# Kernel optimization log

Measured on AMD Instinct MI355X. Metric: run time of the kernel, lower is better.

## Reference

```python
import jax, jax.numpy as jnp
import numpy as np

B, S, H, NH, NKV, HD, E, I = 1, 2048, 1024, 16, 8, 64, 8, 2048
TOPK = 2
EPS = 1e-6
THETA = 1e6


def setup_inputs() -> dict:
    key = jax.random.key(0)
    ks = jax.random.split(key, 12)
    init = lambda k, shp: jax.random.normal(k, shp, jnp.float32) * 0.02
    hidden_states = jax.random.normal(ks[0], (B, S, H), jnp.float32)
    attention_mask = jnp.ones((B, S), jnp.float32)
    position_ids = jnp.broadcast_to(jnp.arange(S, dtype=jnp.int32), (B, S))
    inv_freq = 1.0 / (THETA ** (jnp.arange(0, HD, 2, dtype=jnp.float32) / HD))
    freqs = jnp.outer(jnp.arange(S, dtype=jnp.float32), inv_freq)  # [S, HD/2]
    emb = jnp.concatenate([freqs, freqs], axis=-1)                  # [S, HD]
    return dict(
        hidden_states=hidden_states,
        attention_mask=attention_mask,
        position_ids=position_ids,
        sin=jnp.sin(emb), cos=jnp.cos(emb),
        wq=init(ks[1], (H, NH * HD)),
        wk=init(ks[2], (H, NKV * HD)),
        wv=init(ks[3], (H, NKV * HD)),
        wo=init(ks[4], (NH * HD, H)),
        ln1=jnp.ones((H,), jnp.float32),
        ln2=jnp.ones((H,), jnp.float32),
        gate_w=init(ks[5], (H, E)),
        w1=init(ks[6], (E, H, I)),
        w3=init(ks[7], (E, H, I)),
        w2=init(ks[8], (E, I, H)),
    )


def _rms_norm(x, w):
    return x * jax.lax.rsqrt(jnp.mean(jnp.square(x), -1, keepdims=True) + EPS) * w


def _rotate_half(x):
    h = x.shape[-1] // 2
    return jnp.concatenate([-x[..., h:], x[..., :h]], axis=-1)


def reference(hidden_states, attention_mask, position_ids, sin, cos,
              wq, wk, wv, wo, ln1, ln2, gate_w, w1, w3, w2):
    x = hidden_states
    # ---- self-attention block ----
    h = _rms_norm(x, ln1)
    q = (h @ wq).reshape(B, S, NH, HD).transpose(0, 2, 1, 3)    # [B,NH,S,HD]
    k = (h @ wk).reshape(B, S, NKV, HD).transpose(0, 2, 1, 3)   # [B,NKV,S,HD]
    v = (h @ wv).reshape(B, S, NKV, HD).transpose(0, 2, 1, 3)
    sb = sin[position_ids][:, None]  # [B,1,S,HD]
    cb = cos[position_ids][:, None]
    q = q * cb + _rotate_half(q) * sb
    k = k * cb + _rotate_half(k) * sb
    rep = NH // NKV
    k = jnp.repeat(k, rep, axis=1)  # GQA repeat -> [B,NH,S,HD]
    v = jnp.repeat(v, rep, axis=1)
    causal = jnp.tril(jnp.ones((S, S), bool))
    mask = causal[None, None] & (attention_mask[:, None, None, :] > 0)
    bias = jnp.where(mask, 0.0, jnp.finfo(jnp.float32).min)
    scale = 1.0 / jnp.sqrt(jnp.float32(HD))
    scores = jnp.einsum('bhqd,bhkd->bhqk', q, k) * scale + bias
    attn = jax.nn.softmax(scores, axis=-1)
    o = jnp.einsum('bhqk,bhkd->bhqd', attn, v)
    o = o.transpose(0, 2, 1, 3).reshape(B, S, NH * HD) @ wo
    x = x + o
    # ---- sparse MoE block (top-2 of E experts, SiLU-gated MLP) ----
    t = _rms_norm(x, ln2).reshape(B * S, H)
    router_logits = t @ gate_w                         # [T,E]
    probs = jax.nn.softmax(router_logits, axis=-1)
    top_w, top_i = jax.lax.top_k(probs, TOPK)          # [T,2]
    top_w = top_w / jnp.sum(top_w, axis=-1, keepdims=True)
    full_w = jnp.sum(jax.nn.one_hot(top_i, E, dtype=t.dtype) * top_w[..., None], axis=1)  # [T,E]
    moe_out = jnp.zeros_like(t)
    for e in range(E):  # fixed small expert count
        ge = jax.nn.silu(t @ w1[e]) * (t @ w3[e])      # [T,I]
        moe_out = moe_out + full_w[:, e:e + 1] * (ge @ w2[e])
    x = x + moe_out.reshape(B, S, H)
    return x
```

## Files before the change

### kernel.cpp

```cpp
#include <hip/hip_runtime.h>

#define S 2048
#define H 1024
#define NH 16
#define NKV 8
#define HD 64
#define NE 8
#define ID 2048

typedef short bf16x8 __attribute__((ext_vector_type(8)));
typedef short bf16x4 __attribute__((ext_vector_type(4)));
typedef float f32x4 __attribute__((ext_vector_type(4)));

__device__ __forceinline__ unsigned short f2bf(float f) {
  unsigned u = __builtin_bit_cast(unsigned, f);
  u += 0x7FFFu + ((u >> 16) & 1u);
  return (unsigned short)(u >> 16);
}
__device__ __forceinline__ float bf2f(unsigned short h) {
  unsigned u = ((unsigned)h) << 16;
  return __builtin_bit_cast(float, u);
}
__device__ __forceinline__ unsigned cvtpk(float a, float b) {
  unsigned r;
  asm("v_cvt_pk_bf16_f32 %0, %1, %2" : "=v"(r) : "v"(a), "v"(b));
  return r;
}

typedef const __attribute__((address_space(1))) unsigned int gas_u32;
typedef __attribute__((address_space(3))) unsigned int las_u32;
__device__ __forceinline__ void gload16(const unsigned short* g, unsigned short* l) {
  __builtin_amdgcn_global_load_lds((gas_u32*)g, (las_u32*)l, 16, 0, 0);
}

__global__ __launch_bounds__(256) void rmsnorm_kernel(const float* __restrict__ x,
                                                      const float* __restrict__ wgt,
                                                      unsigned short* __restrict__ ohi,
                                                      unsigned short* __restrict__ olo) {
  int row = blockIdx.x;
  const float* xr = x + (size_t)row * H;
  int tid = threadIdx.x;
  float v[4];
  float ss = 0.f;
#pragma unroll
  for (int i = 0; i < 4; i++) {
    v[i] = xr[tid + i * 256];
    ss += v[i] * v[i];
  }
#pragma unroll
  for (int off = 1; off < 64; off <<= 1) ss += __shfl_xor(ss, off);
  __shared__ float part[4];
  if ((tid & 63) == 0) part[tid >> 6] = ss;
  __syncthreads();
  float tot = part[0] + part[1] + part[2] + part[3];
  float r = rsqrtf(tot * (1.f / H) + 1e-6f);
#pragma unroll
  for (int i = 0; i < 4; i++) {
    int c = tid + i * 256;
    float vv = v[i] * r * wgt[c];
    size_t o = (size_t)row * H + c;
    unsigned short h_ = f2bf(vv);
    ohi[o] = h_;
    olo[o] = f2bf(vv - bf2f(h_));
  }
}

__global__ __launch_bounds__(256) void rmsnorm_router_kernel(
    const float* __restrict__ x, const float* __restrict__ wgt,
    const float* __restrict__ gw, unsigned short* __restrict__ ohi,
    int* __restrict__ selE, float* __restrict__ selW) {
  int row = blockIdx.x;
  const float* xr = x + (size_t)row * H;
  int tid = threadIdx.x;
  float v[4];
  float ss = 0.f;
#pragma unroll
  for (int i = 0; i < 4; i++) {
    v[i] = xr[tid + i * 256];
    ss += v[i] * v[i];
  }
#pragma unroll
  for (int off = 1; off < 64; off <<= 1) ss += __shfl_xor(ss, off);
  __shared__ float part[4];
  __shared__ float red[4][NE];
  if ((tid & 63) == 0) part[tid >> 6] = ss;
  __syncthreads();
  float tot = part[0] + part[1] + part[2] + part[3];
  float r = rsqrtf(tot * (1.f / H) + 1e-6f);
  float acc[NE];
#pragma unroll
  for (int e = 0; e < NE; e++) acc[e] = 0.f;
#pragma unroll
  for (int i = 0; i < 4; i++) {
    int c = tid + i * 256;
    float vv = v[i] * r * wgt[c];
    ohi[(size_t)row * H + c] = f2bf(vv);
    const float4* gp = (const float4*)(gw + (size_t)c * NE);
    float4 g0 = gp[0], g1 = gp[1];
    acc[0] += vv * g0.x;
    acc[1] += vv * g0.y;
    acc[2] += vv * g0.z;
    acc[3] += vv * g0.w;
    acc[4] += vv * g1.x;
    acc[5] += vv * g1.y;
    acc[6] += vv * g1.z;
    acc[7] += vv * g1.w;
  }
#pragma unroll
  for (int off = 1; off < 64; off <<= 1) {
#pragma unroll
    for (int e = 0; e < NE; e++) acc[e] += __shfl_xor(acc[e], off);
  }
  if ((tid & 63) == 0) {
#pragma unroll
    for (int e = 0; e < NE; e++) red[tid >> 6][e] = acc[e];
  }
  __syncthreads();
  if (tid == 0) {
    float lg[NE];
#pragma unroll
    for (int e = 0; e < NE; e++) lg[e] = red[0][e] + red[1][e] + red[2][e] + red[3][e];
    int e1 = 0;
#pragma unroll
    for (int e = 1; e < NE; e++)
      if (lg[e] > lg[e1]) e1 = e;
    int e2 = -1;
#pragma unroll
    for (int e = 0; e < NE; e++)
      if (e != e1 && (e2 < 0 || lg[e] > lg[e2])) e2 = e;
    float w1v = 1.f / (1.f + __expf(lg[e2] - lg[e1]));
    selE[row] = e1 | (e2 << 8);
    selW[row * 2] = w1v;
    selW[row * 2 + 1] = 1.f - w1v;
  }
}

__global__ __launch_bounds__(256) void assign_kernel(const int* __restrict__ selE,
                                                     const float* __restrict__ selW,
                                                     int* __restrict__ cnt,
                                                     int* __restrict__ offs,
                                                     int* __restrict__ tmap,
                                                     int* __restrict__ idxb,
                                                     float* __restrict__ wgtb) {
  int tid = threadIdx.x;
  __shared__ int sc[256][NE];
  int pack[8];
  int hist[NE];
#pragma unroll
  for (int e = 0; e < NE; e++) hist[e] = 0;
#pragma unroll
  for (int i = 0; i < 8; i++) {
    pack[i] = selE[tid * 8 + i];
    hist[pack[i] & 255]++;
    hist[(pack[i] >> 8) & 255]++;
  }
#pragma unroll
  for (int e = 0; e < NE; e++) sc[tid][e] = hist[e];
  __syncthreads();
  for (int off = 1; off < 256; off <<= 1) {
    int add[NE];
    bool has = tid >= off;
    if (has) {
#pragma unroll
      for (int e = 0; e < NE; e++) add[e] = sc[tid - off][e];
    }
    __syncthreads();
    if (has) {
#pragma unroll
      for (int e = 0; e < NE; e++) sc[tid][e] += add[e];
    }
    __syncthreads();
  }
  if (tid == 0) {
    int a = 0, t = 0;
    for (int e = 0; e < NE; e++) {
      int totE = sc[255][e];
      offs[e] = a;
      cnt[e] = totE;
      int nt = (totE + 127) >> 7;
      for (int i = 0; i < nt; i++) tmap[t++] = (e << 16) | i;
      a += totE;
    }
    offs[NE] = a;
    tmap[63] = t;
  }
  int run[NE];
#pragma unroll
  for (int e = 0; e < NE; e++) run[e] = sc[tid][e] - hist[e];
#pragma unroll
  for (int i = 0; i < 8; i++) {
    int tok = tid * 8 + i;
    int e1 = pack[i] & 255, e2 = (pack[i] >> 8) & 255;
    float wa = selW[tok * 2], wb = selW[tok * 2 + 1];
    int p1 = run[e1]++;
    idxb[e1 * S + p1] = tok;
    wgtb[e1 * S + p1] = wa;
    int p2 = run[e2]++;
    idxb[e2 * S + p2] = tok;
    wgtb[e2 * S + p2] = wb;
  }
}

template <bool LO>
__global__ __launch_bounds__(256) void tconv_kernel(const float* __restrict__ src,
                                                    unsigned short* __restrict__ hi,
                                                    unsigned short* __restrict__ lo,
                                                    int K, int N, long long sStride,
                                                    long long dStride) {
  int nt = blockIdx.x, kt = blockIdx.y, b = blockIdx.z;
  src += (size_t)b * sStride;
  hi += (size_t)b * dStride;
  if (LO) lo += (size_t)b * dStride;
  __shared__ float tile[64][65];
  int tid = threadIdx.x;
  int r = tid >> 2, cs = (tid & 3) * 16;
  const float* s0 = src + (size_t)(kt * 64 + r) * N + nt * 64 + cs;
#pragma unroll
  for (int i = 0; i < 16; i += 4) {
    float4 a = *(const float4*)(s0 + i);
    tile[r][cs + i] = a.x;
    tile[r][cs + i + 1] = a.y;
    tile[r][cs + i + 2] = a.z;
    tile[r][cs + i + 3] = a.w;
  }
  __syncthreads();
  int n = nt * 64 + r;
  size_t dbase = (size_t)n * K + kt * 64 + cs;
  unsigned short th[16], tl[16];
#pragma unroll
  for (int i = 0; i < 16; i++) {
    float vv = tile[cs + i][r];
    unsigned short h_ = f2bf(vv);
    th[i] = h_;
    if (LO) tl[i] = f2bf(vv - bf2f(h_));
  }
  *(bf16x8*)(hi + dbase) = *(bf16x8*)&th[0];
  *(bf16x8*)(hi + dbase + 8) = *(bf16x8*)&th[8];
  if (LO) {
    *(bf16x8*)(lo + dbase) = *(bf16x8*)&tl[0];
    *(bf16x8*)(lo + dbase + 8) = *(bf16x8*)&tl[8];
  }
}

template <int MODE>
__global__ __launch_bounds__(256, (MODE >= 2 ? 4 : 3)) void gemm_kernel(
    const unsigned short* __restrict__ Ah, const unsigned short* __restrict__ Al,
    const unsigned short* __restrict__ Bh, const unsigned short* __restrict__ Bl,
    float* __restrict__ C, float* __restrict__ C2, unsigned short* __restrict__ Gout,
    const float* __restrict__ resid, const int* __restrict__ idx,
    const float* __restrict__ wgt, const int* __restrict__ cnt,
    const int* __restrict__ offs, const int* __restrict__ tmap, int N, int K) {
  int n0 = blockIdx.x * 64, m0, e = 0;
  int ce = 0, gbase = 0;
  if (MODE >= 2) {
    int ntiles = tmap[63];
    if ((int)blockIdx.y >= ntiles) return;
    int packed = tmap[blockIdx.y];
    e = packed >> 16;
    m0 = (packed & 0xffff) * 128;
    ce = cnt[e];
    gbase = offs[e];
  } else {
    m0 = blockIdx.y * 128;
  }
  const unsigned short* bhp = Bh;
  const unsigned short* blp = Bl;
  if (MODE == 2) {
    bhp += (size_t)e * 2048 * 1024;
    blp += (size_t)e * 2048 * 1024;
  }
  if (MODE == 3) bhp += (size_t)e * 1024 * 2048;

  __shared__ __align__(16) unsigned short tAh[128 * 64];
  __shared__ __align__(16) unsigned short tAl[MODE <= 1 ? 128 * 64 : 8];
  __shared__ __align__(16) unsigned short tBh[64 * 64];
  __shared__ __align__(16) unsigned short tBl[MODE <= 2 ? 64 * 64 : 8];

  int tid = threadIdx.x, w = tid >> 6, lane = tid & 63;
  int lr = lane & 15, g = lane >> 4;
  int rloc = lane >> 3, slotg = (lane & 7) ^ rloc;
  int wm = w >> 1, wn = w & 1;

  unsigned aOff[4], bOff[2];
#pragma unroll
  for (int cc = 0; cc < 4; cc++) {
    int rr = w * 32 + cc * 8 + rloc;
    if (MODE == 2) {
      int gr = m0 + rr;
      if (gr > ce - 1) gr = ce - 1;
      int tok = idx[e * S + gr];
      aOff[cc] = (unsigned)(tok * K + slotg * 8);
    } else if (MODE == 3) {
      int gr = gbase + m0 + rr;
      if (gr > 4095) gr = 4095;
      aOff[cc] = (unsigned)(gr * K + slotg * 8);
    } else {
      aOff[cc] = (unsigned)((m0 + rr) * K + slotg * 8);
    }
  }
#pragma unroll
  for (int cc = 0; cc < 2; cc++) {
    int rr = w * 16 + cc * 8 + rloc;
    bOff[cc] = (unsigned)((n0 + rr) * K + slotg * 8);
  }

  f32x4 acc[4][2], acc2[4][2];
#pragma unroll
  for (int i = 0; i < 4; i++)
#pragma unroll
    for (int j = 0; j < 2; j++) {
      acc[i][j] = f32x4{0.f, 0.f, 0.f, 0.f};
      if (MODE == 2) acc2[i][j] = f32x4{0.f, 0.f, 0.f, 0.f};
    }

  int kbeg = 0, kend = K;
  if (MODE == 3) {
    kbeg = (int)blockIdx.z * (K >> 1);
    kend = kbeg + (K >> 1);
  }
  for (int k0 = kbeg; k0 < kend; k0 += 64) {
    __syncthreads();
#pragma unroll
    for (int cc = 0; cc < 4; cc++) {
      int cb = (w * 4 + cc) * 512;
      gload16(Ah + aOff[cc] + k0, &tAh[cb]);
      if (MODE <= 1) gload16(Al + aOff[cc] + k0, &tAl[cb]);
    }
#pragma unroll
    for (int cc = 0; cc < 2; cc++) {
      int cb = (w * 2 + cc) * 512;
      gload16(bhp + bOff[cc] + k0, &tBh[cb]);
      if (MODE <= 2) gload16(blp + bOff[cc] + k0, &tBl[cb]);
    }
    __syncthreads();
    bf16x8 fah[4][2], fal[4][2];
#pragma unroll
    for (int i = 0; i < 4; i++) {
      int ar = wm * 64 + i * 16 + lr;
#pragma unroll
      for (int kk = 0; kk < 2; kk++) {
        int off = ar * 64 + (((kk * 4 + g) ^ (ar & 7)) * 8);
        fah[i][kk] = *(const bf16x8*)&tAh[off];
        if (MODE <= 1) fal[i][kk] = *(const bf16x8*)&tAl[off];
      }
    }
#pragma unroll
    for (int j = 0; j < 2; j++) {
      int br = wn * 32 + j * 16 + lr;
      bf16x8 fbh[2], fbl[2];
#pragma unroll
      for (int kk = 0; kk < 2; kk++) {
        int off = br * 64 + (((kk * 4 + g) ^ (br & 7)) * 8);
        fbh[kk] = *(const bf16x8*)&tBh[off];
        if (MODE <= 2) fbl[kk] = *(const bf16x8*)&tBl[off];
      }
#pragma unroll
      for (int i = 0; i < 4; i++) {
#pragma unroll
        for (int kk = 0; kk < 2; kk++) {
          acc[i][j] = __builtin_amdgcn_mfma_f32_16x16x32_bf16(fah[i][kk], fbh[kk], acc[i][j], 0, 0, 0);
          if (MODE <= 1) {
            acc[i][j] = __builtin_amdgcn_mfma_f32_16x16x32_bf16(fah[i][kk], fbl[kk], acc[i][j], 0, 0, 0);
            acc[i][j] = __builtin_amdgcn_mfma_f32_16x16x32_bf16(fal[i][kk], fbh[kk], acc[i][j], 0, 0, 0);
          }
          if (MODE == 2)
            acc2[i][j] = __builtin_amdgcn_mfma_f32_16x16x32_bf16(fah[i][kk], fbl[kk], acc2[i][j], 0, 0, 0);
        }
      }
    }
  }
#pragma unroll
  for (int i = 0; i < 4; i++)
#pragma unroll
    for (int j = 0; j < 2; j++)
#pragma unroll
      for (int r = 0; r < 4; r++) {
        int grow = wm * 64 + i * 16 + g * 4 + r;
        int gcol = n0 + wn * 32 + j * 16 + lr;
        float v = acc[i][j][r];
        if (MODE == 0) {
          C[(size_t)(m0 + grow) * N + gcol] = v;
        } else if (MODE == 1) {
          float o = v + resid[(size_t)(m0 + grow) * N + gcol];
          C[(size_t)(m0 + grow) * N + gcol] = o;
          C2[(size_t)(m0 + grow) * N + gcol] = o;
        } else if (MODE == 2) {
          if (m0 + grow < ce) {
            float g3 = acc2[i][j][r];
            float sg = v / (1.f + __expf(-v));
            Gout[(size_t)(gbase + m0 + grow) * 2048 + gcol] = f2bf(sg * g3);
          }
        } else {
          if (m0 + grow < ce) {
            int tok = idx[e * S + m0 + grow];
            float wv = wgt[e * S + m0 + grow];
            atomicAdd(&C[(size_t)tok * 1024 + gcol], v * wv);
          }
        }
      }
}

__global__ __launch_bounds__(256) void rope_kernel(
    const float* __restrict__ qkv, const float* __restrict__ sinb,
    const float* __restrict__ cosb, const int* __restrict__ pos,
    unsigned short* __restrict__ qhi, unsigned short* __restrict__ qlo,
    unsigned short* __restrict__ khi, unsigned short* __restrict__ klo) {
  int i = blockIdx.x * 256 + threadIdx.x;
  int d = i & 31;
  int s = (i >> 5) & 2047;
  int hh = i >> 16;
  int p = pos[s];
  float c0 = cosb[p * HD + d], c1 = cosb[p * HD + d + 32];
  float s0 = sinb[p * HD + d], s1 = sinb[p * HD + d + 32];
  const float* srcb = qkv + (size_t)s * 2048;
  if (hh < NH) {
    float x0 = srcb[hh * HD + d], x1 = srcb[hh * HD + d + 32];
    float r0 = (x0 * c0 - x1 * s0) * 0.125f;
    float r1 = (x1 * c1 + x0 * s1) * 0.125f;
    size_t o = ((size_t)hh * S + s) * HD + d;
    unsigned short h0 = f2bf(r0), h1 = f2bf(r1);
    qhi[o] = h0;
    qlo[o] = f2bf(r0 - bf2f(h0));
    qhi[o + 32] = h1;
    qlo[o + 32] = f2bf(r1 - bf2f(h1));
  } else {
    int hk = hh - NH;
    float x0 = srcb[1024 + hk * HD + d], x1 = srcb[1024 + hk * HD + d + 32];
    float r0 = x0 * c0 - x1 * s0;
    float r1 = x1 * c1 + x0 * s1;
    size_t o = ((size_t)hk * S + s) * HD + d;
    unsigned short h0 = f2bf(r0), h1 = f2bf(r1);
    khi[o] = h0;
    klo[o] = f2bf(r0 - bf2f(h0));
    khi[o + 32] = h1;
    klo[o + 32] = f2bf(r1 - bf2f(h1));
  }
}

__global__ __launch_bounds__(256) void vtrans_kernel(const float* __restrict__ qkv,
                                                     unsigned short* __restrict__ vThi,
                                                     unsigned short* __restrict__ vTlo) {
  int st = blockIdx.x, hk = blockIdx.y;
  __shared__ float tile[64][65];
  int tid = threadIdx.x;
  int r = tid >> 2, seg = (tid & 3) * 16;
  const float* src = qkv + (size_t)(st * 64 + r) * 2048 + 1536 + hk * HD + seg;
#pragma unroll
  for (int i = 0; i < 16; i += 4) {
    float4 a = *(const float4*)(src + i);
    tile[r][seg + i] = a.x;
    tile[r][seg + i + 1] = a.y;
    tile[r][seg + i + 2] = a.z;
    tile[r][seg + i + 3] = a.w;
  }
  __syncthreads();
  int d = tid >> 2, ss = (tid & 3) * 16;
  unsigned short th[16], tl[16];
#pragma unroll
  for (int i = 0; i < 16; i++) {
    float vv = tile[ss + i][d];
    unsigned short h_ = f2bf(vv);
    th[i] = h_;
    tl[i] = f2bf(vv - bf2f(h_));
  }
  size_t dst = ((size_t)hk * HD + d) * S + st * 64 + ss;
  *(bf16x8*)(vThi + dst) = *(bf16x8*)&th[0];
  *(bf16x8*)(vThi + dst + 8) = *(bf16x8*)&th[8];
  *(bf16x8*)(vTlo + dst) = *(bf16x8*)&tl[0];
  *(bf16x8*)(vTlo + dst + 8) = *(bf16x8*)&tl[8];
}

#define FSWZ(row, byteoff) ((byteoff) ^ (((row) & 7) << 4))

__global__ __launch_bounds__(256, 4) void flash_kernel(
    const unsigned short* __restrict__ qhi, const unsigned short* __restrict__ qlo,
    const unsigned short* __restrict__ khip, const unsigned short* __restrict__ klop,
    const unsigned short* __restrict__ vthip, const unsigned short* __restrict__ vtlop,
    const float* __restrict__ amask, float* __restrict__ po, float* __restrict__ pm,
    float* __restrict__ pl) {
  int u = blockIdx.x;
  int r_ = u >> 8, base = u & 255;
  int qt = (base + r_ * 8) & 31;
  int head = ((base >> 5) & 7) | ((r_ & 1) << 3);
  int z = r_ >> 1;
  int tid = threadIdx.x;
  int w = tid >> 6, lane = tid & 63;
  int lr = lane & 15, g = lane >> 4;
  int rloc = lane >> 3, slotg = (lane & 7) ^ rloc;

  __shared__ __align__(16) unsigned short Khi[64 * 64];
  __shared__ __align__(16) unsigned short Klo[64 * 64];
  __shared__ __align__(16) unsigned short Vhi[64 * 64];
  __shared__ __align__(16) unsigned short Vlo[64 * 64];
  __shared__ __align__(16) unsigned short Pbuf[4][16 * 64];

  int qrow = qt * 64 + w * 16 + lr;
  bf16x8 qh[2], ql[2];
  {
    const unsigned short* qb = qhi + ((size_t)head * S + qrow) * HD;
    const unsigned short* qb2 = qlo + ((size_t)head * S + qrow) * HD;
    qh[0] = *(const bf16x8*)(qb + g * 8);
    qh[1] = *(const bf16x8*)(qb + 32 + g * 8);
    ql[0] = *(const bf16x8*)(qb2 + g * 8);
    ql[1] = *(const bf16x8*)(qb2 + 32 + g * 8);
  }

  f32x4 oacc[4];
#pragma unroll
  for (int dg = 0; dg < 4; dg++) oacc[dg] = f32x4{0.f, 0.f, 0.f, 0.f};
  float m = -1e30f, l = 0.f;

  const unsigned short* kbh = khip + (size_t)(head >> 1) * S * HD;
  const unsigned short* kbl = klop + (size_t)(head >> 1) * S * HD;
  const unsigned short* vbh = vthip + (size_t)(head >> 1) * HD * S;
  const unsigned short* vbl = vtlop + (size_t)(head >> 1) * HD * S;
  char* pbase = (char*)Pbuf[w];

  int nblk = qt + 1;
  int b0 = (z * nblk) >> 1, b1 = ((z + 1) * nblk) >> 1;

  for (int kb = b0; kb < b1; kb++) {
    int kv0 = kb * 64;
    __syncthreads();
#pragma unroll
    for (int cc = 0; cc < 2; cc++) {
      int c = w * 2 + cc;
      int r = c * 8 + rloc;
      gload16(kbh + (size_t)(kv0 + r) * HD + slotg * 8, &Khi[c * 512]);
      gload16(kbl + (size_t)(kv0 + r) * HD + slotg * 8, &Klo[c * 512]);
      gload16(vbh + (size_t)r * S + kv0 + slotg * 8, &Vhi[c * 512]);
      gload16(vbl + (size_t)r * S + kv0 + slotg * 8, &Vlo[c * 512]);
    }
    unsigned long long vm = __ballot(amask[kv0 + lane] > 0.f);
    __syncthreads();

    f32x4 sacc[4];
#pragma unroll
    for (int c = 0; c < 4; c++) sacc[c] = f32x4{0.f, 0.f, 0.f, 0.f};
#pragma unroll
    for (int c = 0; c < 4; c++) {
#pragma unroll
      for (int kc = 0; kc < 2; kc++) {
        int row = c * 16 + lr;
        int bo = FSWZ(row, row * 128 + kc * 64 + g * 16);
        bf16x8 khf = *(const bf16x8*)((char*)Khi + bo);
        bf16x8 klf = *(const bf16x8*)((char*)Klo + bo);
        sacc[c] = __builtin_amdgcn_mfma_f32_16x16x32_bf16(khf, qh[kc], sacc[c], 0, 0, 0);
        sacc[c] = __builtin_amdgcn_mfma_f32_16x16x32_bf16(khf, ql[kc], sacc[c], 0, 0, 0);
        sacc[c] = __builtin_amdgcn_mfma_f32_16x16x32_bf16(klf, qh[kc], sacc[c], 0, 0, 0);
      }
    }
    int qloc = w * 16 + lr;
    bool diag = (kb == qt);
    bool fullvis = (vm == ~0ull) && !diag;
    float tm = -1e30f;
    if (fullvis) {
#pragma unroll
      for (int c = 0; c < 4; c++)
#pragma unroll
        for (int r = 0; r < 4; r++) tm = fmaxf(tm, sacc[c][r]);
    } else {
#pragma unroll
      for (int c = 0; c < 4; c++) {
#pragma unroll
        for (int r = 0; r < 4; r++) {
          int kvloc = c * 16 + 4 * g + r;
          bool vis = ((vm >> kvloc) & 1ull) && (!diag || kvloc <= qloc);
          float sv = vis ? sacc[c][r] : -1e30f;
          sacc[c][r] = sv;
          tm = fmaxf(tm, sv);
        }
      }
    }
    tm = fmaxf(tm, __shfl_xor(tm, 16));
    tm = fmaxf(tm, __shfl_xor(tm, 32));
    bool skip = __all(tm - m <= 8.f);
    float newm = skip ? m : fmaxf(m, tm);
    float rs = 0.f;
#pragma unroll
    for (int c = 0; c < 4; c++) {
#pragma unroll
      for (int r = 0; r < 4; r++) {
        float p = __expf(sacc[c][r] - newm);
        sacc[c][r] = p;
        rs += p;
      }
    }
    rs += __shfl_xor(rs, 16);
    rs += __shfl_xor(rs, 32);
    if (!skip) {
      float alpha = __expf(m - newm);
      m = newm;
      l = l * alpha + rs;
#pragma unroll
      for (int dg = 0; dg < 4; dg++) {
#pragma unroll
        for (int r = 0; r < 4; r++) oacc[dg][r] *= alpha;
      }
    } else {
      l += rs;
    }
    unsigned hw[4][2];
#pragma unroll
    for (int c = 0; c < 4; c++) {
      hw[c][0] = cvtpk(sacc[c][0], sacc[c][1]);
      hw[c][1] = cvtpk(sacc[c][2], sacc[c][3]);
      uint2 hv = {hw[c][0], hw[c][1]};
      *(uint2*)(pbase + FSWZ(lr, lr * 128 + (c * 16 + 4 * g) * 2)) = hv;
    }
    bf16x8 pbh[2], pbl[2];
#pragma unroll
    for (int kc = 0; kc < 2; kc++)
      pbh[kc] = *(const bf16x8*)(pbase + FSWZ(lr, lr * 128 + kc * 64 + g * 16));
#pragma unroll
    for (int c = 0; c < 4; c++) {
      float h0 = __builtin_bit_cast(float, hw[c][0] << 16);
      float h1 = __builtin_bit_cast(float, hw[c][0] & 0xffff0000u);
      float h2 = __builtin_bit_cast(float, hw[c][1] << 16);
      float h3 = __builtin_bit_cast(float, hw[c][1] & 0xffff0000u);
      uint2 lv = {cvtpk(sacc[c][0] - h0, sacc[c][1] - h1),
                  cvtpk(sacc[c][2] - h2, sacc[c][3] - h3)};
      *(uint2*)(pbase + FSWZ(lr, lr * 128 + (c * 16 + 4 * g) * 2)) = lv;
    }
#pragma unroll
    for (int kc = 0; kc < 2; kc++)
      pbl[kc] = *(const bf16x8*)(pbase + FSWZ(lr, lr * 128 + kc * 64 + g * 16));
#pragma unroll
    for (int dg = 0; dg < 4; dg++) {
#pragma unroll
      for (int kc = 0; kc < 2; kc++) {
        int row = dg * 16 + lr;
        int bo = FSWZ(row, row * 128 + kc * 64 + g * 16);
        bf16x8 vhf = *(const bf16x8*)((char*)Vhi + bo);
        bf16x8 vlf = *(const bf16x8*)((char*)Vlo + bo);
        oacc[dg] = __builtin_amdgcn_mfma_f32_16x16x32_bf16(vhf, pbh[kc], oacc[dg], 0, 0, 0);
        oacc[dg] = __builtin_amdgcn_mfma_f32_16x16x32_bf16(vhf, pbl[kc], oacc[dg], 0, 0, 0);
        oacc[dg] = __builtin_amdgcn_mfma_f32_16x16x32_bf16(vlf, pbh[kc], oacc[dg], 0, 0, 0);
      }
    }
  }

  size_t pb = (size_t)(qt * 16 + head) * 2 + z;
  int row = w * 16 + lr;
  if (g == 0) {
    pm[pb * 64 + row] = m;
    pl[pb * 64 + row] = l;
  }
  float* pob = po + pb * 4096 + (size_t)row * 64;
#pragma unroll
  for (int dg = 0; dg < 4; dg++) {
    float4 v4 = {oacc[dg][0], oacc[dg][1], oacc[dg][2], oacc[dg][3]};
    *(float4*)(pob + dg * 16 + 4 * g) = v4;
  }
}

__global__ __launch_bounds__(256) void combine_kernel(const float* __restrict__ po,
                                                      const float* __restrict__ pm,
                                                      const float* __restrict__ pl,
                                                      unsigned short* __restrict__ ohi,
                                                      unsigned short* __restrict__ olo) {
  int qt = blockIdx.x, head = blockIdx.y;
  int r = threadIdx.x >> 2, dg = (threadIdx.x & 3) * 16;
  size_t base = (size_t)(qt * 16 + head) * 2;
  float m0v = pm[base * 64 + r], m1v = pm[(base + 1) * 64 + r];
  float l0 = pl[base * 64 + r], l1 = pl[(base + 1) * 64 + r];
  float M = fmaxf(m0v, m1v);
  float w0 = __expf(m0v - M), w1 = __expf(m1v - M);
  float inv = 1.f / (w0 * l0 + w1 * l1);
  const float* p0 = po + base * 4096 + (size_t)r * 64 + dg;
  const float* p1 = po + (base + 1) * 4096 + (size_t)r * 64 + dg;
  unsigned short th[16], tl[16];
#pragma unroll
  for (int i = 0; i < 16; i += 4) {
    float4 a = *(const float4*)(p0 + i);
    float4 b = *(const float4*)(p1 + i);
    float vv[4] = {(w0 * a.x + w1 * b.x) * inv, (w0 * a.y + w1 * b.y) * inv,
                   (w0 * a.z + w1 * b.z) * inv, (w0 * a.w + w1 * b.w) * inv};
#pragma unroll
    for (int j = 0; j < 4; j++) {
      unsigned short h_ = f2bf(vv[j]);
      th[i + j] = h_;
      tl[i + j] = f2bf(vv[j] - bf2f(h_));
    }
  }
  size_t ob = (size_t)(qt * 64 + r) * 1024 + head * 64 + dg;
  *(bf16x8*)(ohi + ob) = *(bf16x8*)&th[0];
  *(bf16x8*)(ohi + ob + 8) = *(bf16x8*)&th[8];
  *(bf16x8*)(olo + ob) = *(bf16x8*)&tl[0];
  *(bf16x8*)(olo + ob + 8) = *(bf16x8*)&tl[8];
}

extern "C" void kernel_launch(void* const* d_in, const int* in_sizes, int n_in,
                              void* d_out, int out_size, void* d_ws, size_t ws_size,
                              hipStream_t stream) {
  const float* x = (const float*)d_in[0];
  const float* amask = (const float*)d_in[1];
  const int* pos = (const int*)d_in[2];
  const float* sinb = (const float*)d_in[3];
  const float* cosb = (const float*)d_in[4];
  const float* wq = (const float*)d_in[5];
  const float* wk = (const float*)d_in[6];
  const float* wv = (const float*)d_in[7];
  const float* wo = (const float*)d_in[8];
  const float* ln1 = (const float*)d_in[9];
  const float* ln2 = (const float*)d_in[10];
  const float* gw = (const float*)d_in[11];
  const float* w1 = (const float*)d_in[12];
  const float* w3 = (const float*)d_in[13];
  const float* w2 = (const float*)d_in[14];
  float* out = (float*)d_out;

  char* ws = (char*)d_ws;
  const size_t MB = 1024 * 1024;
  float* x2 = (float*)(ws + 0 * MB);
  unsigned short* t_bf = (unsigned short*)(ws + 8 * MB);
  int* cnt = (int*)(ws + 12 * MB);
  int* offs = cnt + 16;
  int* tmap = cnt + 32;
  int* idxb = cnt + 128;
  float* wgtb = (float*)(idxb + NE * S);
  unsigned short* G = (unsigned short*)(ws + 13 * MB);
  unsigned short* w1T = (unsigned short*)(ws + 29 * MB);
  unsigned short* w3T = (unsigned short*)(ws + 61 * MB);
  unsigned short* w2T = (unsigned short*)(ws + 29 * MB);
  float* qkv = (float*)(ws + 13 * MB);
  float* po = (float*)(ws + 13 * MB);
  unsigned short* wqkvT_hi = (unsigned short*)(ws + 29 * MB);
  unsigned short* wqkvT_lo = (unsigned short*)(ws + 33 * MB);
  unsigned short* woT_hi = (unsigned short*)(ws + 37 * MB);
  unsigned short* woT_lo = (unsigned short*)(ws + 39 * MB);
  unsigned short* h_hi = (unsigned short*)(ws + 41 * MB);
  unsigned short* h_lo = (unsigned short*)(ws + 45 * MB);
  unsigned short* q_hi = (unsigned short*)(ws + 49 * MB);
  unsigned short* q_lo = (unsigned short*)(ws + 53 * MB);
  unsigned short* k_hi = (unsigned short*)(ws + 57 * MB);
  unsigned short* k_lo = (unsigned short*)(ws + 59 * MB);
  unsigned short* vT_hi = (unsigned short*)(ws + 61 * MB);
  unsigned short* vT_lo = (unsigned short*)(ws + 63 * MB);
  unsigned short* o_hi = (unsigned short*)(ws + 65 * MB);
  unsigned short* o_lo = (unsigned short*)(ws + 69 * MB);
  float* pm = (float*)(ws + 81 * MB);
  float* pl = (float*)(ws + 82 * MB);
  int* selE = (int*)(ws + 83 * MB);
  float* selW = (float*)(ws + 84 * MB);

  rmsnorm_kernel<<<S, 256, 0, stream>>>(x, ln1, h_hi, h_lo);
  tconv_kernel<true><<<dim3(16, 16, 1), 256, 0, stream>>>(wq, wqkvT_hi, wqkvT_lo, 1024, 1024, 0, 0);
  tconv_kernel<true><<<dim3(8, 16, 1), 256, 0, stream>>>(wk, wqkvT_hi + (size_t)1024 * 1024,
                                                         wqkvT_lo + (size_t)1024 * 1024, 1024, 512, 0, 0);
  tconv_kernel<true><<<dim3(8, 16, 1), 256, 0, stream>>>(wv, wqkvT_hi + (size_t)1536 * 1024,
                                                         wqkvT_lo + (size_t)1536 * 1024, 1024, 512, 0, 0);
  tconv_kernel<true><<<dim3(16, 16, 1), 256, 0, stream>>>(wo, woT_hi, woT_lo, 1024, 1024, 0, 0);

  gemm_kernel<0><<<dim3(32, 16, 1), 256, 0, stream>>>(h_hi, h_lo, wqkvT_hi, wqkvT_lo, qkv, nullptr,
                                                      nullptr, nullptr, nullptr, nullptr, nullptr,
                                                      nullptr, nullptr, 2048, 1024);
  rope_kernel<<<6144, 256, 0, stream>>>(qkv, sinb, cosb, pos, q_hi, q_lo, k_hi, k_lo);
  vtrans_kernel<<<dim3(32, 8), 256, 0, stream>>>(qkv, vT_hi, vT_lo);
  flash_kernel<<<dim3(1024, 1, 1), 256, 0, stream>>>(q_hi, q_lo, k_hi, k_lo, vT_hi, vT_lo, amask,
                                                     po, pm, pl);
  combine_kernel<<<dim3(32, 16), 256, 0, stream>>>(po, pm, pl, o_hi, o_lo);
  gemm_kernel<1><<<dim3(16, 16, 1), 256, 0, stream>>>(o_hi, o_lo, woT_hi, woT_lo, x2, out, nullptr,
                                                      x, nullptr, nullptr, nullptr, nullptr,
                                                      nullptr, 1024, 1024);
  rmsnorm_router_kernel<<<S, 256, 0, stream>>>(x2, ln2, gw, t_bf, selE, selW);
  assign_kernel<<<1, 256, 0, stream>>>(selE, selW, cnt, offs, tmap, idxb, wgtb);

  tconv_kernel<false><<<dim3(32, 16, 8), 256, 0, stream>>>(w1, w1T, nullptr, 1024, 2048,
                                                           (long long)1024 * 2048,
                                                           (long long)2048 * 1024);
  tconv_kernel<false><<<dim3(32, 16, 8), 256, 0, stream>>>(w3, w3T, nullptr, 1024, 2048,
                                                           (long long)1024 * 2048,
                                                           (long long)2048 * 1024);
  gemm_kernel<2><<<dim3(32, 40, 1), 256, 0, stream>>>(t_bf, nullptr, w1T, w3T, nullptr, nullptr, G,
                                                      nullptr, idxb, wgtb, cnt, offs, tmap, 2048,
                                                      1024);
  tconv_kernel<false><<<dim3(16, 32, 8), 256, 0, stream>>>(w2, w2T, nullptr, 2048, 1024,
                                                           (long long)2048 * 1024,
                                                           (long long)1024 * 2048);
  gemm_kernel<3><<<dim3(16, 40, 2), 256, 0, stream>>>(G, nullptr, w2T, nullptr, out, nullptr,
                                                      nullptr, nullptr, idxb, wgtb, cnt, offs, tmap,
                                                      1024, 2048);
}
```

Before: 307.3 us.

## Replace MoE down-proj atomics with slot-indexed partial stores and gather; halve dense GEMM M-tile

The expert down-projection GEMM no longer scatters weighted results into the output with float atomicAdd. It writes unweighted partial results per split-K half into a slot-ordered buffer, and a new gather kernel combines both experts and both K-halves per token, applying the routing weights. The assign kernel now records each token's slot positions instead of per-slot weights. Separately, the dense QKV and output-projection GEMMs use a 64-row M tile with doubled grid and 4-wave occupancy, which adds blocks to improve CU utilisation. The trade-off is an extra kernel launch and a 32MB intermediate buffer round trip in place of the atomic contention.

```diff
diff --git a/kernel.cpp b/kernel.cpp
--- a/kernel.cpp
+++ b/kernel.cpp
@@ -136,12 +136,11 @@
 }
 
 __global__ __launch_bounds__(256) void assign_kernel(const int* __restrict__ selE,
-                                                     const float* __restrict__ selW,
                                                      int* __restrict__ cnt,
                                                      int* __restrict__ offs,
                                                      int* __restrict__ tmap,
                                                      int* __restrict__ idxb,
-                                                     float* __restrict__ wgtb) {
+                                                     int* __restrict__ tokslot) {
   int tid = threadIdx.x;
   __shared__ int sc[256][NE];
   int pack[8];
@@ -171,17 +170,25 @@
     }
     __syncthreads();
   }
+  int offsL[NE];
+  {
+    int a = 0;
+#pragma unroll
+    for (int e = 0; e < NE; e++) {
+      offsL[e] = a;
+      a += sc[255][e];
+    }
+  }
   if (tid == 0) {
-    int a = 0, t = 0;
+    int t = 0;
     for (int e = 0; e < NE; e++) {
       int totE = sc[255][e];
-      offs[e] = a;
+      offs[e] = offsL[e];
       cnt[e] = totE;
       int nt = (totE + 127) >> 7;
       for (int i = 0; i < nt; i++) tmap[t++] = (e << 16) | i;
-      a += totE;
-    }
-    offs[NE] = a;
+    }
+    offs[NE] = offsL[NE - 1] + sc[255][NE - 1];
     tmap[63] = t;
   }
   int run[NE];
@@ -191,14 +198,36 @@
   for (int i = 0; i < 8; i++) {
     int tok = tid * 8 + i;
     int e1 = pack[i] & 255, e2 = (pack[i] >> 8) & 255;
-    float wa = selW[tok * 2], wb = selW[tok * 2 + 1];
     int p1 = run[e1]++;
     idxb[e1 * S + p1] = tok;
-    wgtb[e1 * S + p1] = wa;
     int p2 = run[e2]++;
     idxb[e2 * S + p2] = tok;
-    wgtb[e2 * S + p2] = wb;
-  }
+    tokslot[tok * 2] = offsL[e1] + p1;
+    tokslot[tok * 2 + 1] = offsL[e2] + p2;
+  }
+}
+
+__global__ __launch_bounds__(256) void moe_gather_kernel(const float* __restrict__ moeP,
+                                                         const int* __restrict__ tokslot,
+                                                         const float* __restrict__ selW,
+                                                         float* __restrict__ out) {
+  int tok = blockIdx.x;
+  int c = threadIdx.x * 4;
+  int s0 = tokslot[tok * 2], s1 = tokslot[tok * 2 + 1];
+  float w0 = selW[tok * 2], w1 = selW[tok * 2 + 1];
+  const float* P0 = moeP;
+  const float* P1 = moeP + (size_t)4096 * 1024;
+  float4 a0 = *(const float4*)(P0 + (size_t)s0 * 1024 + c);
+  float4 b0 = *(const float4*)(P1 + (size_t)s0 * 1024 + c);
+  float4 a1 = *(const float4*)(P0 + (size_t)s1 * 1024 + c);
+  float4 b1 = *(const float4*)(P1 + (size_t)s1 * 1024 + c);
+  float* op = out + (size_t)tok * 1024 + c;
+  float4 o = *(float4*)op;
+  o.x += w0 * (a0.x + b0.x) + w1 * (a1.x + b1.x);
+  o.y += w0 * (a0.y + b0.y) + w1 * (a1.y + b1.y);
+  o.z += w0 * (a0.z + b0.z) + w1 * (a1.z + b1.z);
+  o.w += w0 * (a0.w + b0.w) + w1 * (a1.w + b1.w);
+  *(float4*)op = o;
 }
 
 template <bool LO>
@@ -243,13 +272,15 @@
 }
 
 template <int MODE>
-__global__ __launch_bounds__(256, (MODE >= 2 ? 4 : 3)) void gemm_kernel(
+__global__ __launch_bounds__(256, 4) void gemm_kernel(
     const unsigned short* __restrict__ Ah, const unsigned short* __restrict__ Al,
     const unsigned short* __restrict__ Bh, const unsigned short* __restrict__ Bl,
     float* __restrict__ C, float* __restrict__ C2, unsigned short* __restrict__ Gout,
     const float* __restrict__ resid, const int* __restrict__ idx,
-    const float* __restrict__ wgt, const int* __restrict__ cnt,
-    const int* __restrict__ offs, const int* __restrict__ tmap, int N, int K) {
+    const int* __restrict__ cnt, const int* __restrict__ offs,
+    const int* __restrict__ tmap, int N, int K) {
+  constexpr int BM = (MODE <= 1) ? 64 : 128;
+  constexpr int NI = BM / 32;
   int n0 = blockIdx.x * 64, m0, e = 0;
   int ce = 0, gbase = 0;
   if (MODE >= 2) {
@@ -261,7 +292,7 @@
     ce = cnt[e];
     gbase = offs[e];
   } else {
-    m0 = blockIdx.y * 128;
+    m0 = blockIdx.y * BM;
   }
   const unsigned short* bhp = Bh;
   const unsigned short* blp = Bl;
@@ -271,8 +302,8 @@
   }
   if (MODE == 3) bhp += (size_t)e * 1024 * 2048;
 
-  __shared__ __align__(16) unsigned short tAh[128 * 64];
-  __shared__ __align__(16) unsigned short tAl[MODE <= 1 ? 128 * 64 : 8];
+  __shared__ __align__(16) unsigned short tAh[BM * 64];
+  __shared__ __align__(16) unsigned short tAl[MODE <= 1 ? BM * 64 : 8];
   __shared__ __align__(16) unsigned short tBh[64 * 64];
   __shared__ __align__(16) unsigned short tBl[MODE <= 2 ? 64 * 64 : 8];
 
@@ -281,10 +312,10 @@
   int rloc = lane >> 3, slotg = (lane & 7) ^ rloc;
   int wm = w >> 1, wn = w & 1;
 
-  unsigned aOff[4], bOff[2];
-#pragma unroll
-  for (int cc = 0; cc < 4; cc++) {
-    int rr = w * 32 + cc * 8 + rloc;
+  unsigned aOff[NI], bOff[2];
+#pragma unroll
+  for (int cc = 0; cc < NI; cc++) {
+    int rr = (w * NI + cc) * 8 + rloc;
     if (MODE == 2) {
       int gr = m0 + rr;
       if (gr > ce - 1) gr = ce - 1;
@@ -300,13 +331,13 @@
   }
 #pragma unroll
   for (int cc = 0; cc < 2; cc++) {
-    int rr = w * 16 + cc * 8 + rloc;
+    int rr = (w * 2 + cc) * 8 + rloc;
     bOff[cc] = (unsigned)((n0 + rr) * K + slotg * 8);
   }
 
-  f32x4 acc[4][2], acc2[4][2];
-#pragma unroll
-  for (int i = 0; i < 4; i++)
+  f32x4 acc[NI][2], acc2[NI][2];
+#pragma unroll
+  for (int i = 0; i < NI; i++)
 #pragma unroll
     for (int j = 0; j < 2; j++) {
       acc[i][j] = f32x4{0.f, 0.f, 0.f, 0.f};
@@ -321,8 +352,8 @@
   for (int k0 = kbeg; k0 < kend; k0 += 64) {
     __syncthreads();
 #pragma unroll
-    for (int cc = 0; cc < 4; cc++) {
-      int cb = (w * 4 + cc) * 512;
+    for (int cc = 0; cc < NI; cc++) {
+      int cb = (w * NI + cc) * 512;
       gload16(Ah + aOff[cc] + k0, &tAh[cb]);
       if (MODE <= 1) gload16(Al + aOff[cc] + k0, &tAl[cb]);
     }
@@ -333,10 +364,10 @@
       if (MODE <= 2) gload16(blp + bOff[cc] + k0, &tBl[cb]);
     }
     __syncthreads();
-    bf16x8 fah[4][2], fal[4][2];
-#pragma unroll
-    for (int i = 0; i < 4; i++) {
-      int ar = wm * 64 + i * 16 + lr;
+    bf16x8 fah[NI][2], fal[NI][2];
+#pragma unroll
+    for (int i = 0; i < NI; i++) {
+      int ar = wm * (BM / 2) + i * 16 + lr;
 #pragma unroll
       for (int kk = 0; kk < 2; kk++) {
         int off = ar * 64 + (((kk * 4 + g) ^ (ar & 7)) * 8);
@@ -355,7 +386,7 @@
         if (MODE <= 2) fbl[kk] = *(const bf16x8*)&tBl[off];
       }
 #pragma unroll
-      for (int i = 0; i < 4; i++) {
+      for (int i = 0; i < NI; i++) {
 #pragma unroll
         for (int kk = 0; kk < 2; kk++) {
           acc[i][j] = __builtin_amdgcn_mfma_f32_16x16x32_bf16(fah[i][kk], fbh[kk], acc[i][j], 0, 0, 0);
@@ -370,12 +401,12 @@
     }
   }
 #pragma unroll
-  for (int i = 0; i < 4; i++)
+  for (int i = 0; i < NI; i++)
 #pragma unroll
     for (int j = 0; j < 2; j++)
 #pragma unroll
       for (int r = 0; r < 4; r++) {
-        int grow = wm * 64 + i * 16 + g * 4 + r;
+        int grow = wm * (BM / 2) + i * 16 + g * 4 + r;
         int gcol = n0 + wn * 32 + j * 16 + lr;
         float v = acc[i][j][r];
         if (MODE == 0) {
@@ -392,9 +423,7 @@
           }
         } else {
           if (m0 + grow < ce) {
-            int tok = idx[e * S + m0 + grow];
-            float wv = wgt[e * S + m0 + grow];
-            atomicAdd(&C[(size_t)tok * 1024 + gcol], v * wv);
+            C[(size_t)blockIdx.z * 4096 * 1024 + (size_t)(gbase + m0 + grow) * 1024 + gcol] = v;
           }
         }
       }
@@ -718,11 +747,14 @@
   int* offs = cnt + 16;
   int* tmap = cnt + 32;
   int* idxb = cnt + 128;
-  float* wgtb = (float*)(idxb + NE * S);
+  int* selE = idxb + 16384;
+  int* tokslot = selE + 2048;
+  float* selW = (float*)(tokslot + 4096);
   unsigned short* G = (unsigned short*)(ws + 13 * MB);
   unsigned short* w1T = (unsigned short*)(ws + 29 * MB);
   unsigned short* w3T = (unsigned short*)(ws + 61 * MB);
   unsigned short* w2T = (unsigned short*)(ws + 29 * MB);
+  float* moeP = (float*)(ws + 61 * MB);
   float* qkv = (float*)(ws + 13 * MB);
   float* po = (float*)(ws + 13 * MB);
   unsigned short* wqkvT_hi = (unsigned short*)(ws + 29 * MB);
@@ -739,10 +771,8 @@
   unsigned short* vT_lo = (unsigned short*)(ws + 63 * MB);
   unsigned short* o_hi = (unsigned short*)(ws + 65 * MB);
   unsigned short* o_lo = (unsigned short*)(ws + 69 * MB);
-  float* pm = (float*)(ws + 81 * MB);
-  float* pl = (float*)(ws + 82 * MB);
-  int* selE = (int*)(ws + 83 * MB);
-  float* selW = (float*)(ws + 84 * MB);
+  float* pm = (float*)(ws + 73 * MB);
+  float* pl = (float*)(ws + 74 * MB);
 
   rmsnorm_kernel<<<S, 256, 0, stream>>>(x, ln1, h_hi, h_lo);
   tconv_kernel<true><<<dim3(16, 16, 1), 256, 0, stream>>>(wq, wqkvT_hi, wqkvT_lo, 1024, 1024, 0, 0);
@@ -752,19 +782,19 @@
                                                          wqkvT_lo + (size_t)1536 * 1024, 1024, 512, 0, 0);
   tconv_kernel<true><<<dim3(16, 16, 1), 256, 0, stream>>>(wo, woT_hi, woT_lo, 1024, 1024, 0, 0);
 
-  gemm_kernel<0><<<dim3(32, 16, 1), 256, 0, stream>>>(h_hi, h_lo, wqkvT_hi, wqkvT_lo, qkv, nullptr,
+  gemm_kernel<0><<<dim3(32, 32, 1), 256, 0, stream>>>(h_hi, h_lo, wqkvT_hi, wqkvT_lo, qkv, nullptr,
                                                       nullptr, nullptr, nullptr, nullptr, nullptr,
-                                                      nullptr, nullptr, 2048, 1024);
+                                                      nullptr, 2048, 1024);
   rope_kernel<<<6144, 256, 0, stream>>>(qkv, sinb, cosb, pos, q_hi, q_lo, k_hi, k_lo);
   vtrans_kernel<<<dim3(32, 8), 256, 0, stream>>>(qkv, vT_hi, vT_lo);
   flash_kernel<<<dim3(1024, 1, 1), 256, 0, stream>>>(q_hi, q_lo, k_hi, k_lo, vT_hi, vT_lo, amask,
                                                      po, pm, pl);
   combine_kernel<<<dim3(32, 16), 256, 0, stream>>>(po, pm, pl, o_hi, o_lo);
-  gemm_kernel<1><<<dim3(16, 16, 1), 256, 0, stream>>>(o_hi, o_lo, woT_hi, woT_lo, x2, out, nullptr,
-                                                      x, nullptr, nullptr, nullptr, nullptr,
-                                                      nullptr, 1024, 1024);
+  gemm_kernel<1><<<dim3(16, 32, 1), 256, 0, stream>>>(o_hi, o_lo, woT_hi, woT_lo, x2, out, nullptr,
+                                                      x, nullptr, nullptr, nullptr, nullptr, 1024,
+                                                      1024);
   rmsnorm_router_kernel<<<S, 256, 0, stream>>>(x2, ln2, gw, t_bf, selE, selW);
-  assign_kernel<<<1, 256, 0, stream>>>(selE, selW, cnt, offs, tmap, idxb, wgtb);
+  assign_kernel<<<1, 256, 0, stream>>>(selE, cnt, offs, tmap, idxb, tokslot);
 
   tconv_kernel<false><<<dim3(32, 16, 8), 256, 0, stream>>>(w1, w1T, nullptr, 1024, 2048,
                                                            (long long)1024 * 2048,
@@ -773,12 +803,12 @@
                                                            (long long)1024 * 2048,
                                                            (long long)2048 * 1024);
   gemm_kernel<2><<<dim3(32, 40, 1), 256, 0, stream>>>(t_bf, nullptr, w1T, w3T, nullptr, nullptr, G,
-                                                      nullptr, idxb, wgtb, cnt, offs, tmap, 2048,
-                                                      1024);
+                                                      nullptr, idxb, cnt, offs, tmap, 2048, 1024);
   tconv_kernel<false><<<dim3(16, 32, 8), 256, 0, stream>>>(w2, w2T, nullptr, 2048, 1024,
                                                            (long long)2048 * 1024,
                                                            (long long)1024 * 2048);
-  gemm_kernel<3><<<dim3(16, 40, 2), 256, 0, stream>>>(G, nullptr, w2T, nullptr, out, nullptr,
-                                                      nullptr, nullptr, idxb, wgtb, cnt, offs, tmap,
-                                                      1024, 2048);
-}
+  gemm_kernel<3><<<dim3(16, 40, 2), 256, 0, stream>>>(G, nullptr, w2T, nullptr, moeP, nullptr,
+                                                      nullptr, nullptr, idxb, cnt, offs, tmap, 1024,
+                                                      2048);
+  moe_gather_kernel<<<S, 256, 0, stream>>>(moeP, tokslot, selW, out);
+}
```

Result: faster. 300.0 us (median of 2 runs) (-2.4%).
